# Performance work log

Hardware: AMD Instinct MI355X
Metric: run time of the kernel (lower is better)

## Reference

```python
import jax, jax.numpy as jnp
import numpy as np

MAX_STEPS = 8
COMMIT = 0.25
DECAY = 0.99
EPS = 1e-5


def gru_cell(x, h, W_ih, W_hh, b_ih, b_hh):
    # PyTorch GRU cell, gate order (r, z, n)
    gx = x @ W_ih.T + b_ih            # [B, 3H]
    gh = h @ W_hh.T + b_hh            # [B, 3H]
    xr, xz, xn = jnp.split(gx, 3, axis=-1)
    hr, hz, hn = jnp.split(gh, 3, axis=-1)
    r = jax.nn.sigmoid(xr + hr)
    z = jax.nn.sigmoid(xz + hz)
    n = jnp.tanh(xn + r * hn)
    return (1.0 - z) * n + z * h


def setup_inputs() -> dict:
    key = jax.random.key(0)
    ks = jax.random.split(key, 16)
    B, C, Hs, Ws = 1024, 512, 7, 7
    D, K, Hd = 256, 8192, 512
    sc = lambda k, shape, s: (jax.random.normal(k, shape, jnp.float32) * s)
    codebook = jax.random.uniform(ks[14], (K, D), jnp.float32, -1.0 / K, 1.0 / K)
    return {
        "spatial_features": sc(ks[0], (B, C, Hs, Ws), 1.0),
        "bos_token": sc(ks[1], (D,), 0.02),
        "W_ih": sc(ks[2], (3 * Hd, D), 0.05),
        "W_hh": sc(ks[3], (3 * Hd, Hd), 0.05),
        "b_ih": sc(ks[4], (3 * Hd,), 0.05),
        "b_hh": sc(ks[5], (3 * Hd,), 0.05),
        "Wg": sc(ks[6], (C, Hd), 0.02),
        "bg": sc(ks[7], (C,), 0.02),
        "Wb": sc(ks[8], (C, Hd), 0.02),
        "bb": sc(ks[9], (C,), 0.02),
        "W1": sc(ks[10], (Hd, Hd + C), 0.03),
        "b1": sc(ks[11], (Hd,), 0.03),
        "W2": sc(ks[12], (D, Hd), 0.05),
        "b2": sc(ks[13], (D,), 0.05),
        "codebook": codebook,
        "ema_cluster_size": jnp.zeros((K,), jnp.float32),
        "ema_w": codebook,
    }


def reference(spatial_features, bos_token, W_ih, W_hh, b_ih, b_hh,
              Wg, bg, Wb, bb, W1, b1, W2, b2,
              codebook, ema_cluster_size, ema_w):
    B = spatial_features.shape[0]
    K, D = codebook.shape
    Hd = W_hh.shape[1]
    # FiLM + global mean pooling is linear -> fold mean over HxW once.
    # mean((1+g)*F + b) == (1+g)*mean(F) + b  (same math, fewer bytes)
    spatial_mean = spatial_features.mean(axis=(2, 3))  # [B, C]

    def step(carry, _):
        h, prev, cb, cs, ew, loss = carry
        h = gru_cell(prev, h, W_ih, W_hh, b_ih, b_hh)            # [B, Hd]
        gamma = h @ Wg.T + bg
        beta = h @ Wb.T + bb
        c = (1.0 + gamma) * spatial_mean + beta                   # [B, C]
        pin = jnp.concatenate([h, c], axis=-1)                    # [B, Hd+C]
        z = jax.nn.relu(pin @ W1.T + b1) @ W2.T + b2              # [B, D]
        # VQ nearest neighbor (squared L2)
        d = (jnp.sum(z * z, axis=-1, keepdims=True)
             - 2.0 * (z @ cb.T)
             + jnp.sum(cb * cb, axis=-1))                         # [B, K]
        idx = jnp.argmin(d, axis=-1)                              # [B]
        z_q = cb[idx]                                             # [B, D]
        # EMA codebook update (uses OLD codebook for this step's z_q)
        zd = jax.lax.stop_gradient(z)
        counts = jnp.zeros((K,), z.dtype).at[idx].add(1.0)
        dw = jnp.zeros_like(cb).at[idx].add(zd)
        cs = DECAY * cs + (1.0 - DECAY) * counts
        n_tot = cs.sum()
        cs = (cs + EPS) / (n_tot + K * EPS) * n_tot               # Laplace smoothing
        ew = DECAY * ew + (1.0 - DECAY) * dw
        cb_new = ew / cs[:, None]
        vq = COMMIT * jnp.mean((z - jax.lax.stop_gradient(z_q)) ** 2)
        z_q_ste = z + jax.lax.stop_gradient(z_q - z)              # straight-through
        return (h, z_q_ste, cb_new, cs, ew, loss + vq), (z_q_ste, idx, z)

    h0 = jnp.zeros((B, Hd), spatial_features.dtype)
    prev0 = jnp.broadcast_to(bos_token, (B, D))
    init = (h0, prev0, codebook, ema_cluster_size, ema_w, jnp.zeros((), jnp.float32))
    (h_final, _, _, _, _, total_loss), (codes, idxs, zc) = jax.lax.scan(
        step, init, None, length=MAX_STEPS)
    selected_codes = jnp.swapaxes(codes, 0, 1)   # [B, T, D]
    all_indices = jnp.swapaxes(idxs, 0, 1)       # [B, T]
    all_z_cont = jnp.swapaxes(zc, 0, 1)          # [B, T, D]
    avg_vq_loss = total_loss / MAX_STEPS
    return (h_final, selected_codes, all_indices, all_z_cont, avg_vq_loss)
```

## Files before the change

### kernel.cpp

```cpp
#include <hip/hip_runtime.h>

#define BATCH 1024
#define CDIM  512
#define DDIM  256
#define KCB   8192
#define HD    512
#define G3    1536
#define TSTEPS 8

#define WS_CB    ((size_t)0)
#define WS_EW    ((size_t)2097152)
#define WS_CSR   ((size_t)4194304)
#define WS_SM    ((size_t)6291456)
#define WS_H     ((size_t)6815744)
#define WS_PREV  ((size_t)7340032)
#define WS_Z     ((size_t)7602176)
#define WS_GX    ((size_t)7864320)
#define WS_GH    ((size_t)9437184)
#define WS_GB    ((size_t)11010048)
#define WS_PIN   ((size_t)12058624)
#define WS_H1    ((size_t)13107200)
#define WS_CS    ((size_t)13631488)
#define WS_CBSQ  ((size_t)13639680)
#define WS_SZZ   ((size_t)13647872)
#define WS_NT    ((size_t)13657088)
#define WS_LOSS  ((size_t)13657090)
#define WS_IDX   ((size_t)13657092)
#define WS_ROWK  ((size_t)13658116)
#define WS_WGWB  ((size_t)13660164)
#define WS_BGBB  ((size_t)14184452)

#define OUT_HF    ((size_t)0)
#define OUT_CODES ((size_t)524288)
#define OUT_IDX   ((size_t)2621440)
#define OUT_ZC    ((size_t)2629632)
#define OUT_LOSS  ((size_t)4726784)

static __device__ __forceinline__ unsigned long long key32(float s, int col) {
  unsigned int u = __float_as_uint(s);
  u = (u & 0x80000000u) ? ~u : (u | 0x80000000u);
  return (((unsigned long long)u) << 32) | (unsigned long long)(unsigned int)col;
}

static __device__ __forceinline__ float pw128(const float* a) {
  float r0=a[0],r1=a[1],r2=a[2],r3=a[3],r4=a[4],r5=a[5],r6=a[6],r7=a[7];
  for (int i = 8; i < 128; i += 8) {
    r0+=a[i+0]; r1+=a[i+1]; r2+=a[i+2]; r3+=a[i+3];
    r4+=a[i+4]; r5+=a[i+5]; r6+=a[i+6]; r7+=a[i+7];
  }
  return ((r0+r1)+(r2+r3))+((r4+r5)+(r6+r7));
}

template<int BM,int BN,int BK,int TM,int TN>
__device__ __forceinline__ void gemm_engine(
    const float* __restrict__ A, int lda,
    const float* __restrict__ B, int ldb, int K,
    int m0, int n0, int tid,
    float* __restrict__ As, float* __restrict__ Bs,
    float (&acc)[TM][TN])
{
  constexpr int NT = 256;
  constexpr int K4 = BK/4;
  constexpr int LA = (BM*BK)/(4*NT);
  constexpr int LB = (BN*BK)/(4*NT);
  constexpr int SA = BM+4;
  constexpr int SB = BN+4;
  static_assert((BM/TM)*(BN/TN) == NT, "256 threads");
  static_assert(LA >= 1 && LB >= 1, "stage width");

  const int tx = tid % (BN/TN);
  const int ty = tid / (BN/TN);

  int arow[LA], ak4[LA], brow[LB], bk4[LB];
#pragma unroll
  for (int l=0;l<LA;++l){ int f=l*NT+tid; arow[l]=f/K4; ak4[l]=f%K4; }
#pragma unroll
  for (int l=0;l<LB;++l){ int f=l*NT+tid; brow[l]=f/K4; bk4[l]=f%K4; }

  float4 ra[LA], rb[LB];
#pragma unroll
  for (int l=0;l<LA;++l) ra[l] = *(const float4*)(A + (size_t)(m0+arow[l])*lda + ak4[l]*4);
#pragma unroll
  for (int l=0;l<LB;++l) rb[l] = *(const float4*)(B + (size_t)(n0+brow[l])*ldb + bk4[l]*4);
#pragma unroll
  for (int l=0;l<LA;++l){ int kb=ak4[l]*4, r=arow[l];
    As[(kb+0)*SA+r]=ra[l].x; As[(kb+1)*SA+r]=ra[l].y; As[(kb+2)*SA+r]=ra[l].z; As[(kb+3)*SA+r]=ra[l].w; }
#pragma unroll
  for (int l=0;l<LB;++l){ int kb=bk4[l]*4, r=brow[l];
    Bs[(kb+0)*SB+r]=rb[l].x; Bs[(kb+1)*SB+r]=rb[l].y; Bs[(kb+2)*SB+r]=rb[l].z; Bs[(kb+3)*SB+r]=rb[l].w; }
  __syncthreads();

  int cur = 0;
  for (int k0 = BK; k0 < K; k0 += BK) {
#pragma unroll
    for (int l=0;l<LA;++l) ra[l] = *(const float4*)(A + (size_t)(m0+arow[l])*lda + k0 + ak4[l]*4);
#pragma unroll
    for (int l=0;l<LB;++l) rb[l] = *(const float4*)(B + (size_t)(n0+brow[l])*ldb + k0 + bk4[l]*4);
    {
      const float* as = As + cur*(BK*SA) + ty*TM;
      const float* bs = Bs + cur*(BK*SB) + tx*TN;
#pragma unroll
      for (int kk=0;kk<BK;++kk){
        float af[TM], bf[TN];
#pragma unroll
        for (int i=0;i<TM;++i) af[i]=as[kk*SA+i];
#pragma unroll
        for (int j=0;j<TN;++j) bf[j]=bs[kk*SB+j];
#pragma unroll
        for (int i=0;i<TM;++i)
#pragma unroll
          for (int j=0;j<TN;++j) acc[i][j]=fmaf(af[i],bf[j],acc[i][j]);
      }
    }
    {
      float* as = As + (cur^1)*(BK*SA);
      float* bs = Bs + (cur^1)*(BK*SB);
#pragma unroll
      for (int l=0;l<LA;++l){ int kb=ak4[l]*4, r=arow[l];
        as[(kb+0)*SA+r]=ra[l].x; as[(kb+1)*SA+r]=ra[l].y; as[(kb+2)*SA+r]=ra[l].z; as[(kb+3)*SA+r]=ra[l].w; }
#pragma unroll
      for (int l=0;l<LB;++l){ int kb=bk4[l]*4, r=brow[l];
        bs[(kb+0)*SB+r]=rb[l].x; bs[(kb+1)*SB+r]=rb[l].y; bs[(kb+2)*SB+r]=rb[l].z; bs[(kb+3)*SB+r]=rb[l].w; }
    }
    __syncthreads();
    cur ^= 1;
  }
  {
    const float* as = As + cur*(BK*SA) + ty*TM;
    const float* bs = Bs + cur*(BK*SB) + tx*TN;
#pragma unroll
    for (int kk=0;kk<BK;++kk){
      float af[TM], bf[TN];
#pragma unroll
      for (int i=0;i<TM;++i) af[i]=as[kk*SA+i];
#pragma unroll
      for (int j=0;j<TN;++j) bf[j]=bs[kk*SB+j];
#pragma unroll
      for (int i=0;i<TM;++i)
#pragma unroll
        for (int j=0;j<TN;++j) acc[i][j]=fmaf(af[i],bf[j],acc[i][j]);
    }
  }
}

__global__ __launch_bounds__(256) void gemm_gxgh_kernel(
    const float* __restrict__ PREV, const float* __restrict__ H,
    const float* __restrict__ Wih, const float* __restrict__ Whh,
    const float* __restrict__ bih, const float* __restrict__ bhh,
    float* __restrict__ GX, float* __restrict__ GH)
{
  __shared__ float As[2*16*(64+4)];
  __shared__ float Bs[2*16*(64+4)];
  const int z = blockIdx.z;
  const float* A   = z ? H   : PREV;
  const float* B   = z ? Whh : Wih;
  const float* bia = z ? bhh : bih;
  float* C         = z ? GH  : GX;
  const int lda    = z ? HD  : DDIM;
  const int m0 = blockIdx.x * 64, n0 = blockIdx.y * 64;
  float acc[4][4] = {};
  gemm_engine<64,64,16,4,4>(A, lda, B, lda, lda, m0, n0, threadIdx.x, As, Bs, acc);
  {
#pragma clang fp contract(off)
    const int tx = threadIdx.x & 15, ty = threadIdx.x >> 4;
#pragma unroll
    for (int i = 0; i < 4; ++i)
#pragma unroll
      for (int j = 0; j < 4; ++j)
        C[(size_t)(m0 + ty*4 + i) * G3 + n0 + tx*4 + j] = acc[i][j] + bia[n0 + tx*4 + j];
  }
}

__global__ __launch_bounds__(256) void gemm_gb_film_kernel(
    const float* __restrict__ H, const float* __restrict__ W,
    const float* __restrict__ bv, const float* __restrict__ SM,
    float* __restrict__ PIN)
{
  __shared__ float As[2*32*(32+4)];
  __shared__ float Bs[2*32*(64+4)];
  const int m0 = blockIdx.x * 32, n0 = blockIdx.y * 64;
  float acc[2][4] = {};
  gemm_engine<32,64,32,2,4>(H, HD, W, HD, HD, m0, n0, threadIdx.x, As, Bs, acc);
  {
#pragma clang fp contract(off)
    const int tx = threadIdx.x & 15, ty = threadIdx.x >> 4;
    const int cb0 = n0 + tx * 4;
#pragma unroll
    for (int i = 0; i < 2; ++i) {
      const int row = m0 + ty*2 + i;
#pragma unroll
      for (int p = 0; p < 2; ++p) {
        float g  = acc[i][2*p]   + bv[cb0 + 2*p];
        float be = acc[i][2*p+1] + bv[cb0 + 2*p + 1];
        const int ch = (cb0 >> 1) + p;
        float t1 = 1.0f + g;
        float t2 = t1 * SM[(size_t)row * CDIM + ch];
        PIN[(size_t)row * 1024 + 512 + ch] = t2 + be;
      }
    }
  }
}

template<bool RELU>
__global__ __launch_bounds__(256) void gemm_mlp_kernel(
    const float* __restrict__ A, int lda,
    const float* __restrict__ B,
    const float* __restrict__ bias, int K, int N, float* __restrict__ C)
{
  __shared__ float As[2*32*(32+4)];
  __shared__ float Bs[2*32*(32+4)];
  const int m0 = blockIdx.x * 32, n0 = blockIdx.y * 32;
  float acc[2][2] = {};
  gemm_engine<32,32,32,2,2>(A, lda, B, K, K, m0, n0, threadIdx.x, As, Bs, acc);
  {
#pragma clang fp contract(off)
    const int tx = threadIdx.x & 15, ty = threadIdx.x >> 4;
#pragma unroll
    for (int i = 0; i < 2; ++i)
#pragma unroll
      for (int j = 0; j < 2; ++j) {
        float v = acc[i][j] + bias[n0 + tx*2 + j];
        if (RELU) v = fmaxf(v, 0.0f);
        C[(size_t)(m0 + ty*2 + i) * N + n0 + tx*2 + j] = v;
      }
  }
}

__global__ __launch_bounds__(256) void gemm_score_argmin(
    const float* __restrict__ Z,
    const float* __restrict__ CBm,
    const float* __restrict__ cbsq,
    const float* __restrict__ szz,
    unsigned long long* __restrict__ rowkeys)
{
  __shared__ float As[2*16*(128+4)];
  __shared__ float Bs[2*16*(128+4)];
  __shared__ unsigned long long Ks[128][17];
  const int tid = threadIdx.x;
  const int m0 = blockIdx.x * 128, n0 = blockIdx.y * 128;
  float acc[8][8] = {};
  gemm_engine<128,128,16,8,8>(Z, DDIM, CBm, DDIM, DDIM, m0, n0, tid, As, Bs, acc);
  {
#pragma clang fp contract(off)
    const int tx = tid & 15, ty = tid >> 4;
    const int nb = n0 + tx * 8;
#pragma unroll
    for (int i = 0; i < 8; ++i) {
      const int row = ty*8 + i;
      const float sz = szz[m0 + row];
      unsigned long long kb[8];
#pragma unroll
      for (int j = 0; j < 8; ++j) {
        float g2 = 2.0f * acc[i][j];
        float t1 = sz - g2;
        float d  = t1 + cbsq[nb + j];
        kb[j] = key32(d, nb + j);
      }
      unsigned long long a0 = kb[0] < kb[1] ? kb[0] : kb[1];
      unsigned long long a1 = kb[2] < kb[3] ? kb[2] : kb[3];
      unsigned long long a2 = kb[4] < kb[5] ? kb[4] : kb[5];
      unsigned long long a3 = kb[6] < kb[7] ? kb[6] : kb[7];
      unsigned long long b0 = a0 < a1 ? a0 : a1;
      unsigned long long b1 = a2 < a3 ? a2 : a3;
      Ks[row][tx] = b0 < b1 ? b0 : b1;
    }
  }
  __syncthreads();
  if (tid < 128) {
    unsigned long long best = Ks[tid][0];
#pragma unroll
    for (int t = 1; t < 16; ++t) {
      unsigned long long v = Ks[tid][t];
      best = v < best ? v : best;
    }
    atomicMin(&rowkeys[m0 + tid], best);
  }
}

__global__ __launch_bounds__(256) void pw256_rows_kernel(const float* __restrict__ src,
                                                         float* __restrict__ dst,
                                                         int square) {
#pragma clang fp contract(off)
  int gid = blockIdx.x * 256 + threadIdx.x;
  int row = gid >> 4;
  int l = gid & 15;
  const float* a = src + (size_t)row * 256 + ((l >> 3) << 7) + (l & 7);
  float v0 = a[0];
  float r = square ? v0 * v0 : v0;
  for (int i = 1; i < 16; ++i) {
    float w = a[i << 3];
    r += square ? w * w : w;
  }
  float t = r + __shfl_xor(r, 1);
  t = t + __shfl_xor(t, 2);
  t = t + __shfl_xor(t, 4);
  float s = t + __shfl_xor(t, 8);
  if (l == 0) dst[row] = s;
}

__global__ __launch_bounds__(256) void smean_kernel(const float* __restrict__ sf,
                                                    float* __restrict__ sm) {
#pragma clang fp contract(off)
  int i = blockIdx.x * 256 + threadIdx.x;
  const float* a = sf + (size_t)i * 49;
  float r0=a[0],r1=a[1],r2=a[2],r3=a[3],r4=a[4],r5=a[5],r6=a[6],r7=a[7];
  for (int k = 8; k < 48; k += 8) {
    r0+=a[k+0]; r1+=a[k+1]; r2+=a[k+2]; r3+=a[k+3];
    r4+=a[k+4]; r5+=a[k+5]; r6+=a[k+6]; r7+=a[k+7];
  }
  float res = ((r0+r1)+(r2+r3))+((r4+r5)+(r6+r7));
  res += a[48];
  sm[i] = res / 49.0f;
}

__global__ __launch_bounds__(256) void previnit_kernel(const float* __restrict__ bos,
                                                       float* __restrict__ prev) {
  int i = blockIdx.x * 256 + threadIdx.x;
  prev[i] = bos[i & (DDIM - 1)];
}

__global__ __launch_bounds__(256) void interleave_film_kernel(
    const float* __restrict__ Wg, const float* __restrict__ Wb,
    const float* __restrict__ bg, const float* __restrict__ bb,
    float* __restrict__ W, float* __restrict__ bv) {
  int i = blockIdx.x * 256 + threadIdx.x;
  int row = i >> 9, k = i & 511;
  const float* src = (row & 1) ? Wb : Wg;
  W[i] = src[(size_t)(row >> 1) * 512 + k];
  if (i < 1024) bv[i] = ((i & 1) ? bb : bg)[i >> 1];
}

__global__ __launch_bounds__(256) void gru_kernel(const float* __restrict__ gx,
                                                  const float* __restrict__ gh,
                                                  float* __restrict__ h,
                                                  float* __restrict__ pin) {
#pragma clang fp contract(off)
  int i = blockIdx.x * 256 + threadIdx.x;
  int b = i >> 9, j = i & 511;
  size_t o = (size_t)b * G3;
  float xr = gx[o + j], xz = gx[o + 512 + j], xn = gx[o + 1024 + j];
  float hr = gh[o + j], hz = gh[o + 512 + j], hn = gh[o + 1024 + j];
  float ar = xr + hr;
  float az = xz + hz;
  float er = expf(-ar);
  float ez = expf(-az);
  float r  = 1.0f / (1.0f + er);
  float zz = 1.0f / (1.0f + ez);
  float rh = r * hn;
  float an = xn + rh;
  float n  = tanhf(an);
  float hold = h[i];
  float t1 = (1.0f - zz) * n;
  float t2 = zz * hold;
  float hnew = t1 + t2;
  h[i] = hnew;
  pin[(size_t)b * 1024 + j] = hnew;
}

__global__ __launch_bounds__(256) void vq_apply_kernel(
    unsigned long long* __restrict__ rowkeys,
    const float* __restrict__ cb, const float* __restrict__ zbuf,
    float* __restrict__ prev, int* __restrict__ idxarr,
    float* __restrict__ loss_acc, float* __restrict__ out, int t)
{
#pragma clang fp contract(off)
  int b = blockIdx.x, d = threadIdx.x;
  int idx = (int)(rowkeys[b] & 0xFFFFFFFFull);
  float zq = cb[(size_t)idx * DDIM + d];
  float zb = zbuf[(size_t)b * DDIM + d];
  float delta = zq - zb;
  float zste = zb + delta;
  size_t td = ((size_t)b * TSTEPS + t) * DDIM + d;
  out[OUT_CODES + td] = zste;
  out[OUT_ZC + td] = zb;
  prev[(size_t)b * DDIM + d] = zste;
  if (d == 0) {
    idxarr[b] = idx;
    out[OUT_IDX + (size_t)b * TSTEPS + t] = (float)idx;
  }
  float diff = zb - zq;
  __shared__ float red[256];
  red[d] = diff * diff; __syncthreads();
  for (int s = 128; s > 0; s >>= 1) { if (d < s) red[d] += red[d + s]; __syncthreads(); }
  if (d == 0) {
    atomicAdd(loss_acc, red[0]);
    rowkeys[b] = ~0ULL;
  }
}

__global__ __launch_bounds__(1024) void csr_build_kernel(const int* __restrict__ idxarr,
                                                         int* __restrict__ list,
                                                         int* __restrict__ base,
                                                         int* __restrict__ cnts) {
  __shared__ int sidx[BATCH];
  __shared__ int scnt[KCB];
  __shared__ int spart[1024];
  const int t = threadIdx.x;
  sidx[t] = idxarr[t];
  for (int i = t; i < KCB; i += 1024) scnt[i] = 0;
  __syncthreads();
  const int my = sidx[t];
  atomicAdd(&scnt[my], 1);
  int rank = 0;
  for (int b = 0; b < t; ++b) rank += (sidx[b] == my) ? 1 : 0;
  __syncthreads();
  const int c0 = t * 8;
  int loc[8]; int s0 = 0;
#pragma unroll
  for (int i = 0; i < 8; ++i) { loc[i] = s0; s0 += scnt[c0 + i]; }
  spart[t] = s0;
  __syncthreads();
  if (t == 0) {
    int run = 0;
    for (int i = 0; i < 1024; ++i) { int v = spart[i]; spart[i] = run; run += v; }
  }
  __syncthreads();
  const int off = spart[t];
#pragma unroll
  for (int i = 0; i < 8; ++i) { base[c0 + i] = off + loc[i]; cnts[c0 + i] = scnt[c0 + i]; }
  const int kb = my >> 3, kr = my & 7;
  int bb = spart[kb];
  for (int i = 0; i < kr; ++i) bb += scnt[(kb << 3) + i];
  list[bb + rank] = t;
}

__global__ __launch_bounds__(256) void cs_fused_kernel(float* __restrict__ cs,
                                                       const int* __restrict__ cnts,
                                                       float* __restrict__ nt) {
#pragma clang fp contract(off)
  __shared__ float scs[KCB];
  __shared__ float s64v[64];
  const int t = threadIdx.x;
  for (int i = t; i < KCB; i += 256) {
    float a = 0.99f * cs[i];
    float b = 0.01f * (float)cnts[i];
    scs[i] = a + b;
  }
  __syncthreads();
  if (t < 64) s64v[t] = pw128(scs + t * 128);
  __syncthreads();
  if (t == 0) {
    float v[64];
    for (int i = 0; i < 64; ++i) v[i] = s64v[i];
    for (int len = 64; len > 1; len >>= 1)
      for (int i = 0; i < (len >> 1); ++i) v[i] = v[2*i] + v[2*i+1];
    nt[0] = v[0];
    s64v[0] = v[0];
  }
  __syncthreads();
  const float n = s64v[0];
  const float den = n + 0.08192f;
  for (int i = t; i < KCB; i += 256) {
    float t1 = scs[i] + 1e-5f;
    float q = t1 / den;
    cs[i] = q * n;
  }
}

__global__ __launch_bounds__(256) void ema_fused_kernel(
    float* __restrict__ ew, const int* __restrict__ list,
    const int* __restrict__ base, const int* __restrict__ cnts,
    const float* __restrict__ zbuf, const float* __restrict__ cs,
    float* __restrict__ cb, float* __restrict__ cbsq)
{
#pragma clang fp contract(off)
  __shared__ float row2[256];
  __shared__ float ch[16];
  const int d = threadIdx.x;
  for (int r = 0; r < 8; ++r) {
    const int k = blockIdx.x * 8 + r;
    const int start = base[k], cnt = cnts[k];
    float acc = 0.0f;
    int i = 0;
    for (; i + 16 <= cnt; i += 16) {
      int bi[16];
#pragma unroll
      for (int u = 0; u < 16; ++u) bi[u] = list[start + i + u];
      float v[16];
#pragma unroll
      for (int u = 0; u < 16; ++u) v[u] = zbuf[(size_t)bi[u] * DDIM + d];
#pragma unroll
      for (int u = 0; u < 16; ++u) acc += v[u];
    }
    for (; i < cnt; ++i) {
      acc += zbuf[(size_t)list[start + i] * DDIM + d];
    }
    const size_t o = (size_t)k * DDIM + d;
    float a = 0.99f * ew[o];
    float bb = 0.01f * acc;
    float e = a + bb;
    ew[o] = e;
    float c = e / cs[k];
    cb[o] = c;
    row2[d] = c * c;
    __syncthreads();
    if (d < 16) {
      int h = d >> 3, j = d & 7;
      const float* p = row2 + h * 128 + j;
      float rr = p[0];
      for (int i2 = 1; i2 < 16; ++i2) rr += p[8 * i2];
      ch[d] = rr;
    }
    __syncthreads();
    if (d == 0) {
      float s0 = ((ch[0]+ch[1])+(ch[2]+ch[3]))+((ch[4]+ch[5])+(ch[6]+ch[7]));
      float s1 = ((ch[8]+ch[9])+(ch[10]+ch[11]))+((ch[12]+ch[13])+(ch[14]+ch[15]));
      cbsq[k] = s0 + s1;
    }
    __syncthreads();
  }
}

__global__ __launch_bounds__(256) void hfinal_kernel(const float* __restrict__ h,
                                                     float* __restrict__ out) {
  int i = blockIdx.x * 256 + threadIdx.x;
  out[OUT_HF + i] = h[i];
}

__global__ void loss_kernel(const float* __restrict__ loss_acc,
                            float* __restrict__ out) {
  out[OUT_LOSS] = 0.25f * (*loss_acc) / ((float)(BATCH * DDIM)) / (float)TSTEPS;
}

extern "C" void kernel_launch(void* const* d_in, const int* in_sizes, int n_in,
                              void* d_out, int out_size, void* d_ws, size_t ws_size,
                              hipStream_t stream) {
  const float* sf    = (const float*)d_in[0];
  const float* bos   = (const float*)d_in[1];
  const float* W_ih  = (const float*)d_in[2];
  const float* W_hh  = (const float*)d_in[3];
  const float* b_ih  = (const float*)d_in[4];
  const float* b_hh  = (const float*)d_in[5];
  const float* Wg    = (const float*)d_in[6];
  const float* bg    = (const float*)d_in[7];
  const float* Wb    = (const float*)d_in[8];
  const float* bb    = (const float*)d_in[9];
  const float* W1    = (const float*)d_in[10];
  const float* b1    = (const float*)d_in[11];
  const float* W2    = (const float*)d_in[12];
  const float* b2    = (const float*)d_in[13];
  const float* cb_in = (const float*)d_in[14];
  const float* cs_in = (const float*)d_in[15];
  const float* ew_in = (const float*)d_in[16];

  float* ws  = (float*)d_ws;
  float* out = (float*)d_out;

  float* CB   = ws + WS_CB;
  float* EW   = ws + WS_EW;
  int*   LIST = (int*)(ws + WS_CSR);
  int*   BASE = LIST + BATCH;
  int*   CNTS = BASE + KCB;
  float* SM   = ws + WS_SM;
  float* H    = ws + WS_H;
  float* PREV = ws + WS_PREV;
  float* Z    = ws + WS_Z;
  float* GX   = ws + WS_GX;
  float* GH   = ws + WS_GH;
  float* PIN  = ws + WS_PIN;
  float* H1   = ws + WS_H1;
  float* CS   = ws + WS_CS;
  float* CBSQ = ws + WS_CBSQ;
  float* SZZ  = ws + WS_SZZ;
  float* NT   = ws + WS_NT;
  float* LOSS = ws + WS_LOSS;
  int*   IDX  = (int*)(ws + WS_IDX);
  unsigned long long* ROWK = (unsigned long long*)(ws + WS_ROWK);
  float* WGWB = ws + WS_WGWB;
  float* BGBB = ws + WS_BGBB;

  (void)hipMemcpyAsync(CB, cb_in, (size_t)KCB * DDIM * 4, hipMemcpyDeviceToDevice, stream);
  (void)hipMemcpyAsync(EW, ew_in, (size_t)KCB * DDIM * 4, hipMemcpyDeviceToDevice, stream);
  (void)hipMemcpyAsync(CS, cs_in, (size_t)KCB * 4, hipMemcpyDeviceToDevice, stream);
  interleave_film_kernel<<<(1024*512)/256, 256, 0, stream>>>(Wg, Wb, bg, bb, WGWB, BGBB);
  (void)hipMemsetAsync(H, 0, (size_t)BATCH * HD * 4, stream);
  (void)hipMemsetAsync(LOSS, 0, 8, stream);
  (void)hipMemsetAsync(ROWK, 0xFF, BATCH * 8, stream);
  previnit_kernel<<<BATCH * DDIM / 256, 256, 0, stream>>>(bos, PREV);
  smean_kernel<<<BATCH * CDIM / 256, 256, 0, stream>>>(sf, SM);
  pw256_rows_kernel<<<(KCB * 16) / 256, 256, 0, stream>>>(CB, CBSQ, 1);

  for (int t = 0; t < TSTEPS; ++t) {
    gemm_gxgh_kernel<<<dim3(BATCH/64, G3/64, 2), 256, 0, stream>>>(
        PREV, H, W_ih, W_hh, b_ih, b_hh, GX, GH);
    gru_kernel<<<BATCH * HD / 256, 256, 0, stream>>>(GX, GH, H, PIN);

    gemm_gb_film_kernel<<<dim3(BATCH/32, 1024/64), 256, 0, stream>>>(H, WGWB, BGBB, SM, PIN);

    gemm_mlp_kernel<true ><<<dim3(BATCH/32, HD/32),  256, 0, stream>>>(PIN, 1024, W1, b1, 1024, HD, H1);
    gemm_mlp_kernel<false><<<dim3(BATCH/32, DDIM/32),256, 0, stream>>>(H1, HD, W2, b2, HD, DDIM, Z);

    pw256_rows_kernel<<<(BATCH * 16) / 256, 256, 0, stream>>>(Z, SZZ, 1);
    gemm_score_argmin<<<dim3(BATCH/128, KCB/128), 256, 0, stream>>>(Z, CB, CBSQ, SZZ, ROWK);
    vq_apply_kernel<<<BATCH, 256, 0, stream>>>(ROWK, CB, Z, PREV, IDX, LOSS, out, t);

    csr_build_kernel<<<1, 1024, 0, stream>>>(IDX, LIST, BASE, CNTS);
    cs_fused_kernel<<<1, 256, 0, stream>>>(CS, CNTS, NT);
    ema_fused_kernel<<<KCB/8, 256, 0, stream>>>(EW, LIST, BASE, CNTS, Z, CS, CB, CBSQ);
  }

  hfinal_kernel<<<BATCH * HD / 256, 256, 0, stream>>>(H, out);
  loss_kernel<<<1, 1, 0, stream>>>(LOSS, out);
}
```

Measured before the change: 2.174 ms.

## Vectorize GEMM shared-memory reads, retile score/MLP GEMMs, fuse CSR and EMA-count kernels

The shared GEMM engine now reads its A and B fragments from LDS as float4/float2 using a strided per-thread layout, in place of scalar loads. The codebook score GEMM moves to 128x64 tiles and does its per-row argmin with wavefront shuffles instead of an LDS table, and the first MLP GEMM uses 64x32 tiles. The CSR build swaps its serial prefix scan for a parallel scan, vectorizes the rank count, and absorbs the cluster-size EMA kernel, removing one launch per step. Together these target LDS instruction count, serial single-thread work, and launch overhead, at the cost of extra barriers and changed output index mappings.

```diff
diff --git a/kernel.cpp b/kernel.cpp
--- a/kernel.cpp
+++ b/kernel.cpp
@@ -17,7 +17,6 @@
 #define WS_Z     ((size_t)7602176)
 #define WS_GX    ((size_t)7864320)
 #define WS_GH    ((size_t)9437184)
-#define WS_GB    ((size_t)11010048)
 #define WS_PIN   ((size_t)12058624)
 #define WS_H1    ((size_t)13107200)
 #define WS_CS    ((size_t)13631488)
@@ -65,6 +64,12 @@
   constexpr int LB = (BN*BK)/(4*NT);
   constexpr int SA = BM+4;
   constexpr int SB = BN+4;
+  constexpr int ACW = (TM % 4 == 0) ? 4 : 2;
+  constexpr int BCW = (TN % 4 == 0) ? 4 : 2;
+  constexpr int ANC = TM/ACW;
+  constexpr int BNC = TN/BCW;
+  constexpr int AR  = BM/ANC;
+  constexpr int BR  = BN/BNC;
   static_assert((BM/TM)*(BN/TN) == NT, "256 threads");
   static_assert(LA >= 1 && LB >= 1, "stage width");
 
@@ -97,15 +102,31 @@
 #pragma unroll
     for (int l=0;l<LB;++l) rb[l] = *(const float4*)(B + (size_t)(n0+brow[l])*ldb + k0 + bk4[l]*4);
     {
-      const float* as = As + cur*(BK*SA) + ty*TM;
-      const float* bs = Bs + cur*(BK*SB) + tx*TN;
+      const float* as = As + cur*(BK*SA);
+      const float* bs = Bs + cur*(BK*SB);
 #pragma unroll
       for (int kk=0;kk<BK;++kk){
         float af[TM], bf[TN];
 #pragma unroll
-        for (int i=0;i<TM;++i) af[i]=as[kk*SA+i];
-#pragma unroll
-        for (int j=0;j<TN;++j) bf[j]=bs[kk*SB+j];
+        for (int c=0;c<ANC;++c){
+          if constexpr (ACW == 4) {
+            float4 v = *(const float4*)&as[kk*SA + c*AR + ty*4];
+            af[c*4+0]=v.x; af[c*4+1]=v.y; af[c*4+2]=v.z; af[c*4+3]=v.w;
+          } else {
+            float2 v = *(const float2*)&as[kk*SA + c*AR + ty*2];
+            af[c*2+0]=v.x; af[c*2+1]=v.y;
+          }
+        }
+#pragma unroll
+        for (int c=0;c<BNC;++c){
+          if constexpr (BCW == 4) {
+            float4 v = *(const float4*)&bs[kk*SB + c*BR + tx*4];
+            bf[c*4+0]=v.x; bf[c*4+1]=v.y; bf[c*4+2]=v.z; bf[c*4+3]=v.w;
+          } else {
+            float2 v = *(const float2*)&bs[kk*SB + c*BR + tx*2];
+            bf[c*2+0]=v.x; bf[c*2+1]=v.y;
+          }
+        }
 #pragma unroll
         for (int i=0;i<TM;++i)
 #pragma unroll
@@ -126,15 +147,31 @@
     cur ^= 1;
   }
   {
-    const float* as = As + cur*(BK*SA) + ty*TM;
-    const float* bs = Bs + cur*(BK*SB) + tx*TN;
+    const float* as = As + cur*(BK*SA);
+    const float* bs = Bs + cur*(BK*SB);
 #pragma unroll
     for (int kk=0;kk<BK;++kk){
       float af[TM], bf[TN];
 #pragma unroll
-      for (int i=0;i<TM;++i) af[i]=as[kk*SA+i];
-#pragma unroll
-      for (int j=0;j<TN;++j) bf[j]=bs[kk*SB+j];
+      for (int c=0;c<ANC;++c){
+        if constexpr (ACW == 4) {
+          float4 v = *(const float4*)&as[kk*SA + c*AR + ty*4];
+          af[c*4+0]=v.x; af[c*4+1]=v.y; af[c*4+2]=v.z; af[c*4+3]=v.w;
+        } else {
+          float2 v = *(const float2*)&as[kk*SA + c*AR + ty*2];
+          af[c*2+0]=v.x; af[c*2+1]=v.y;
+        }
+      }
+#pragma unroll
+      for (int c=0;c<BNC;++c){
+        if constexpr (BCW == 4) {
+          float4 v = *(const float4*)&bs[kk*SB + c*BR + tx*4];
+          bf[c*4+0]=v.x; bf[c*4+1]=v.y; bf[c*4+2]=v.z; bf[c*4+3]=v.w;
+        } else {
+          float2 v = *(const float2*)&bs[kk*SB + c*BR + tx*2];
+          bf[c*2+0]=v.x; bf[c*2+1]=v.y;
+        }
+      }
 #pragma unroll
       for (int i=0;i<TM;++i)
 #pragma unroll
@@ -201,28 +238,35 @@
   }
 }
 
-template<bool RELU>
+template<bool RELU,int BM,int BN,int BK,int TM,int TN>
 __global__ __launch_bounds__(256) void gemm_mlp_kernel(
     const float* __restrict__ A, int lda,
     const float* __restrict__ B,
     const float* __restrict__ bias, int K, int N, float* __restrict__ C)
 {
-  __shared__ float As[2*32*(32+4)];
-  __shared__ float Bs[2*32*(32+4)];
-  const int m0 = blockIdx.x * 32, n0 = blockIdx.y * 32;
-  float acc[2][2] = {};
-  gemm_engine<32,32,32,2,2>(A, lda, B, K, K, m0, n0, threadIdx.x, As, Bs, acc);
-  {
-#pragma clang fp contract(off)
-    const int tx = threadIdx.x & 15, ty = threadIdx.x >> 4;
-#pragma unroll
-    for (int i = 0; i < 2; ++i)
-#pragma unroll
-      for (int j = 0; j < 2; ++j) {
-        float v = acc[i][j] + bias[n0 + tx*2 + j];
+  __shared__ float As[2*BK*(BM+4)];
+  __shared__ float Bs[2*BK*(BN+4)];
+  const int m0 = blockIdx.x * BM, n0 = blockIdx.y * BN;
+  float acc[TM][TN] = {};
+  gemm_engine<BM,BN,BK,TM,TN>(A, lda, B, K, K, m0, n0, threadIdx.x, As, Bs, acc);
+  {
+#pragma clang fp contract(off)
+    constexpr int ACW = (TM % 4 == 0) ? 4 : 2;
+    constexpr int BCW = (TN % 4 == 0) ? 4 : 2;
+    constexpr int AR  = BM/(TM/ACW);
+    constexpr int BR  = BN/(TN/BCW);
+    const int tx = threadIdx.x % (BN/TN), ty = threadIdx.x / (BN/TN);
+#pragma unroll
+    for (int i = 0; i < TM; ++i) {
+      const int row = m0 + (i/ACW)*AR + ty*ACW + (i%ACW);
+#pragma unroll
+      for (int j = 0; j < TN; ++j) {
+        const int col = n0 + (j/BCW)*BR + tx*BCW + (j%BCW);
+        float v = acc[i][j] + bias[col];
         if (RELU) v = fmaxf(v, 0.0f);
-        C[(size_t)(m0 + ty*2 + i) * N + n0 + tx*2 + j] = v;
+        C[(size_t)row * N + col] = v;
       }
+    }
   }
 }
 
@@ -234,23 +278,22 @@
     unsigned long long* __restrict__ rowkeys)
 {
   __shared__ float As[2*16*(128+4)];
-  __shared__ float Bs[2*16*(128+4)];
-  __shared__ unsigned long long Ks[128][17];
+  __shared__ float Bs[2*16*(64+4)];
   const int tid = threadIdx.x;
-  const int m0 = blockIdx.x * 128, n0 = blockIdx.y * 128;
-  float acc[8][8] = {};
-  gemm_engine<128,128,16,8,8>(Z, DDIM, CBm, DDIM, DDIM, m0, n0, tid, As, Bs, acc);
+  const int m0 = blockIdx.x * 128, n0 = blockIdx.y * 64;
+  float acc[8][4] = {};
+  gemm_engine<128,64,16,8,4>(Z, DDIM, CBm, DDIM, DDIM, m0, n0, tid, As, Bs, acc);
   {
 #pragma clang fp contract(off)
     const int tx = tid & 15, ty = tid >> 4;
-    const int nb = n0 + tx * 8;
+    const int nb = n0 + tx * 4;
 #pragma unroll
     for (int i = 0; i < 8; ++i) {
-      const int row = ty*8 + i;
+      const int row = (i >> 2)*64 + ty*4 + (i & 3);
       const float sz = szz[m0 + row];
-      unsigned long long kb[8];
-#pragma unroll
-      for (int j = 0; j < 8; ++j) {
+      unsigned long long kb[4];
+#pragma unroll
+      for (int j = 0; j < 4; ++j) {
         float g2 = 2.0f * acc[i][j];
         float t1 = sz - g2;
         float d  = t1 + cbsq[nb + j];
@@ -258,22 +301,14 @@
       }
       unsigned long long a0 = kb[0] < kb[1] ? kb[0] : kb[1];
       unsigned long long a1 = kb[2] < kb[3] ? kb[2] : kb[3];
-      unsigned long long a2 = kb[4] < kb[5] ? kb[4] : kb[5];
-      unsigned long long a3 = kb[6] < kb[7] ? kb[6] : kb[7];
-      unsigned long long b0 = a0 < a1 ? a0 : a1;
-      unsigned long long b1 = a2 < a3 ? a2 : a3;
-      Ks[row][tx] = b0 < b1 ? b0 : b1;
-    }
-  }
-  __syncthreads();
-  if (tid < 128) {
-    unsigned long long best = Ks[tid][0];
-#pragma unroll
-    for (int t = 1; t < 16; ++t) {
-      unsigned long long v = Ks[tid][t];
-      best = v < best ? v : best;
-    }
-    atomicMin(&rowkeys[m0 + tid], best);
+      unsigned long long best = a0 < a1 ? a0 : a1;
+#pragma unroll
+      for (int mask = 1; mask < 16; mask <<= 1) {
+        unsigned long long o = __shfl_xor(best, mask);
+        best = o < best ? o : best;
+      }
+      if (tx == 0) atomicMin(&rowkeys[m0 + row], best);
+    }
   }
 }
 
@@ -388,13 +423,17 @@
   }
 }
 
-__global__ __launch_bounds__(1024) void csr_build_kernel(const int* __restrict__ idxarr,
-                                                         int* __restrict__ list,
-                                                         int* __restrict__ base,
-                                                         int* __restrict__ cnts) {
-  __shared__ int sidx[BATCH];
+__global__ __launch_bounds__(1024) void csr_cs_kernel(const int* __restrict__ idxarr,
+                                                      int* __restrict__ list,
+                                                      int* __restrict__ base,
+                                                      int* __restrict__ cnts,
+                                                      float* __restrict__ cs,
+                                                      float* __restrict__ nt) {
+  __shared__ __align__(16) int sidx[BATCH];
   __shared__ int scnt[KCB];
   __shared__ int spart[1024];
+  __shared__ float scs[KCB];
+  __shared__ float s64v[64];
   const int t = threadIdx.x;
   sidx[t] = idxarr[t];
   for (int i = t; i < KCB; i += 1024) scnt[i] = 0;
@@ -402,7 +441,14 @@
   const int my = sidx[t];
   atomicAdd(&scnt[my], 1);
   int rank = 0;
-  for (int b = 0; b < t; ++b) rank += (sidx[b] == my) ? 1 : 0;
+  {
+    int b = 0;
+    for (; b + 4 <= t; b += 4) {
+      int4 v = *(const int4*)&sidx[b];
+      rank += (v.x == my) + (v.y == my) + (v.z == my) + (v.w == my);
+    }
+    for (; b < t; ++b) rank += (sidx[b] == my) ? 1 : 0;
+  }
   __syncthreads();
   const int c0 = t * 8;
   int loc[8]; int s0 = 0;
@@ -410,11 +456,18 @@
   for (int i = 0; i < 8; ++i) { loc[i] = s0; s0 += scnt[c0 + i]; }
   spart[t] = s0;
   __syncthreads();
-  if (t == 0) {
-    int run = 0;
-    for (int i = 0; i < 1024; ++i) { int v = spart[i]; spart[i] = run; run += v; }
-  }
-  __syncthreads();
+  for (int off = 1; off < 1024; off <<= 1) {
+    int v = (t >= off) ? spart[t - off] : 0;
+    __syncthreads();
+    spart[t] += v;
+    __syncthreads();
+  }
+  {
+    int incl = spart[t];
+    __syncthreads();
+    spart[t] = incl - s0;
+    __syncthreads();
+  }
   const int off = spart[t];
 #pragma unroll
   for (int i = 0; i < 8; ++i) { base[c0 + i] = off + loc[i]; cnts[c0 + i] = scnt[c0 + i]; }
@@ -422,38 +475,33 @@
   int bb = spart[kb];
   for (int i = 0; i < kr; ++i) bb += scnt[(kb << 3) + i];
   list[bb + rank] = t;
-}
-
-__global__ __launch_bounds__(256) void cs_fused_kernel(float* __restrict__ cs,
-                                                       const int* __restrict__ cnts,
-                                                       float* __restrict__ nt) {
-#pragma clang fp contract(off)
-  __shared__ float scs[KCB];
-  __shared__ float s64v[64];
-  const int t = threadIdx.x;
-  for (int i = t; i < KCB; i += 256) {
-    float a = 0.99f * cs[i];
-    float b = 0.01f * (float)cnts[i];
-    scs[i] = a + b;
-  }
-  __syncthreads();
-  if (t < 64) s64v[t] = pw128(scs + t * 128);
-  __syncthreads();
-  if (t == 0) {
-    float v[64];
-    for (int i = 0; i < 64; ++i) v[i] = s64v[i];
-    for (int len = 64; len > 1; len >>= 1)
-      for (int i = 0; i < (len >> 1); ++i) v[i] = v[2*i] + v[2*i+1];
-    nt[0] = v[0];
-    s64v[0] = v[0];
-  }
-  __syncthreads();
-  const float n = s64v[0];
-  const float den = n + 0.08192f;
-  for (int i = t; i < KCB; i += 256) {
-    float t1 = scs[i] + 1e-5f;
-    float q = t1 / den;
-    cs[i] = q * n;
+
+  {
+#pragma clang fp contract(off)
+    for (int i = t; i < KCB; i += 1024) {
+      float a = 0.99f * cs[i];
+      float b2 = 0.01f * (float)scnt[i];
+      scs[i] = a + b2;
+    }
+    __syncthreads();
+    if (t < 64) s64v[t] = pw128(scs + t * 128);
+    __syncthreads();
+    if (t == 0) {
+      float v[64];
+      for (int i = 0; i < 64; ++i) v[i] = s64v[i];
+      for (int len = 64; len > 1; len >>= 1)
+        for (int i = 0; i < (len >> 1); ++i) v[i] = v[2*i] + v[2*i+1];
+      nt[0] = v[0];
+      s64v[0] = v[0];
+    }
+    __syncthreads();
+    const float n = s64v[0];
+    const float den = n + 0.08192f;
+    for (int i = t; i < KCB; i += 1024) {
+      float t1 = scs[i] + 1e-5f;
+      float q = t1 / den;
+      cs[i] = q * n;
+    }
   }
 }
 
@@ -587,15 +635,14 @@
 
     gemm_gb_film_kernel<<<dim3(BATCH/32, 1024/64), 256, 0, stream>>>(H, WGWB, BGBB, SM, PIN);
 
-    gemm_mlp_kernel<true ><<<dim3(BATCH/32, HD/32),  256, 0, stream>>>(PIN, 1024, W1, b1, 1024, HD, H1);
-    gemm_mlp_kernel<false><<<dim3(BATCH/32, DDIM/32),256, 0, stream>>>(H1, HD, W2, b2, HD, DDIM, Z);
+    gemm_mlp_kernel<true, 64,32,32,4,2><<<dim3(BATCH/64, HD/32),   256, 0, stream>>>(PIN, 1024, W1, b1, 1024, HD, H1);
+    gemm_mlp_kernel<false,32,32,32,2,2><<<dim3(BATCH/32, DDIM/32), 256, 0, stream>>>(H1, HD, W2, b2, HD, DDIM, Z);
 
     pw256_rows_kernel<<<(BATCH * 16) / 256, 256, 0, stream>>>(Z, SZZ, 1);
-    gemm_score_argmin<<<dim3(BATCH/128, KCB/128), 256, 0, stream>>>(Z, CB, CBSQ, SZZ, ROWK);
+    gemm_score_argmin<<<dim3(BATCH/128, KCB/64), 256, 0, stream>>>(Z, CB, CBSQ, SZZ, ROWK);
     vq_apply_kernel<<<BATCH, 256, 0, stream>>>(ROWK, CB, Z, PREV, IDX, LOSS, out, t);
 
-    csr_build_kernel<<<1, 1024, 0, stream>>>(IDX, LIST, BASE, CNTS);
-    cs_fused_kernel<<<1, 256, 0, stream>>>(CS, CNTS, NT);
+    csr_cs_kernel<<<1, 1024, 0, stream>>>(IDX, LIST, BASE, CNTS, CS, NT);
     ema_fused_kernel<<<KCB/8, 256, 0, stream>>>(EW, LIST, BASE, CNTS, Z, CS, CB, CBSQ);
   }
 
```

Result: slower. 2.388 ms (+9.8%).
